# Kernel optimization log

Hardware: AMD Instinct MI355X
Metric: run time of the kernel (lower is better)

## Reference

```python
import jax, jax.numpy as jnp
import numpy as np

CAPS = 16          # num_capsules
DIM = 16           # capsule_dim
NUM_ROUTING = 3
L2_EPS = 1e-12     # tf.nn.l2_normalize epsilon


def setup_inputs() -> dict:
    key = jax.random.key(0)
    k1, k2 = jax.random.split(key)
    inputs = jax.random.normal(k1, (16, 64, 64, 128), dtype=jnp.float32)
    # Conv2D kernel, HWIO layout, fan-in scaled like glorot-ish init
    kernel = jax.random.normal(k2, (3, 3, 128, CAPS * DIM), dtype=jnp.float32) * 0.03
    bias = jnp.zeros((CAPS * DIM,), dtype=jnp.float32)
    return {"inputs": inputs, "kernel": kernel, "bias": bias}


def reference(inputs, kernel, bias):
    # Conv2D(caps*dim, 3x3, padding='same', activation='relu'), channels_last
    x = jax.lax.conv_general_dilated(
        inputs, kernel, window_strides=(1, 1), padding="SAME",
        dimension_numbers=("NHWC", "HWIO", "NHWC"))
    x = jax.nn.relu(x + bias)
    B, H, W, _ = x.shape
    x = x.reshape(B, H * W, CAPS, DIM)            # (B, N, C, D)
    b = jnp.zeros((B, H * W, CAPS), dtype=x.dtype)
    v = None
    for _ in range(NUM_ROUTING):
        c = jax.nn.softmax(b, axis=-1)             # over capsules
        s = jnp.einsum("bnc,bncd->bcd", c, x)      # weighted sum over spatial
        # tf.nn.l2_normalize along last axis
        v = s * jax.lax.rsqrt(jnp.maximum(jnp.sum(s * s, axis=-1, keepdims=True), L2_EPS))
        b = b + jnp.einsum("bncd,bcd->bnc", x, v)  # agreement update
    # tile v over spatial dims: (B,1,1,C*D) -> (B,H,W,C*D)
    out = jnp.broadcast_to(v.reshape(B, 1, 1, CAPS * DIM), (B, H, W, CAPS * DIM))
    return out
```

## Files before the change

kernel.cpp:

```cpp
#include <hip/hip_runtime.h>
#include <hip/hip_bf16.h>

typedef unsigned short u16;
typedef unsigned int   u32;

typedef __bf16 bf16x8 __attribute__((ext_vector_type(8)));
typedef float  f32x4  __attribute__((ext_vector_type(4)));

#define GLDS(gp, lp) __builtin_amdgcn_global_load_lds( \
    (const __attribute__((address_space(1))) void*)(gp), \
    (__attribute__((address_space(3))) void*)(lp), 16, 0, 0)

__device__ __forceinline__ u16 f2b(float f) {
    __hip_bfloat16 h = __float2bfloat16(f);
    u16 u; __builtin_memcpy(&u, &h, 2); return u;
}
__device__ __forceinline__ float blo(u32 u) { return __uint_as_float(u << 16); }
__device__ __forceinline__ float bhi(u32 u) { return __uint_as_float(u & 0xffff0000u); }

__global__ void k_prep(const float* __restrict__ in, const float* __restrict__ wk,
                       u16* __restrict__ pad, u16* __restrict__ BF,
                       float* __restrict__ stats) {
    int bx = blockIdx.x, tid = threadIdx.x;
    if (bx < 4356) {
        int idx = bx * 256 + tid;
        int e0  = idx * 8;
        int ch  = e0 & 127;
        int rest = e0 >> 7;
        int pw = rest % 66;
        int r2 = rest / 66;
        int ph = r2 % 66;
        int b  = r2 / 66;
        u16 ov[8];
        if (ph >= 1 && ph <= 64 && pw >= 1 && pw <= 64) {
            const float* src = in + (((b * 64 + (ph - 1)) * 64 + (pw - 1)) * 128 + ch);
            const float4* s4 = (const float4*)src;
            float4 f0 = s4[0], f1 = s4[1];
            ov[0]=f2b(f0.x); ov[1]=f2b(f0.y); ov[2]=f2b(f0.z); ov[3]=f2b(f0.w);
            ov[4]=f2b(f1.x); ov[5]=f2b(f1.y); ov[6]=f2b(f1.z); ov[7]=f2b(f1.w);
        } else {
            #pragma unroll
            for (int j = 0; j < 8; ++j) ov[j] = 0;
        }
        uint4 w; __builtin_memcpy(&w, ov, 16);
        *(uint4*)(pad + e0) = w;
    } else if (bx < 5508) {
        int t = (bx - 4356) * 256 + tid;
        int j  = t & 7;
        int n  = (t >> 3) & 255;
        int q  = (t >> 11) & 3;
        int kk = (t >> 13) & 3;
        int p  = t >> 15;
        BF[t] = f2b(wk[(p * 128 + kk * 32 + q * 8 + j) * 256 + n]);
    } else {
        stats[(bx - 5508) * 256 + tid] = 0.f;
    }
}

__launch_bounds__(256, 2)
__global__ void k_conv(const u16* __restrict__ Ap, const u16* __restrict__ BF,
                       const float* __restrict__ bias,
                       u16* __restrict__ X, float* __restrict__ s0) {
    __shared__ u16 ldsA[25344];
    const int t = threadIdx.x;
    const int lane = t & 63, wid = t >> 6;
    const int q = lane >> 4, l15 = lane & 15;
    const int bb = blockIdx.x >> 6;
    const int h  = blockIdx.x & 63;
    const int wn0 = wid << 6;

    const int sbase0 = wid * 792;
    #pragma unroll
    for (int i = 0; i < 12; ++i) {
        int sb = sbase0 + i * 64;
        int slot = sb + lane;
        int r = slot / 1056, rem = slot - r * 1056;
        int w = rem >> 4, cs = rem & 15;
        int c = cs ^ (w & 15);
        const u16* g = Ap + ((((bb * 66 + h + r) * 66 + w) << 7) + (c << 3));
        GLDS(g, (char*)ldsA + sb * 16);
    }
    {
        int sb = sbase0 + 768;
        if (lane < 24) {
            int slot = sb + lane;
            int r = slot / 1056, rem = slot - r * 1056;
            int w = rem >> 4, cs = rem & 15;
            int c = cs ^ (w & 15);
            const u16* g = Ap + ((((bb * 66 + h + r) * 66 + w) << 7) + (c << 3));
            GLDS(g, (char*)ldsA + sb * 16);
        }
    }
    __syncthreads();

    const u16* BFl = BF + (q * 2048 + (wn0 + l15) * 8);

    f32x4 zero = {0.f, 0.f, 0.f, 0.f};
    f32x4 acc[4][4];
    #pragma unroll
    for (int mi = 0; mi < 4; ++mi)
        #pragma unroll
        for (int ni = 0; ni < 4; ++ni) acc[mi][ni] = zero;

#define LOADB(B, P) { \
    _Pragma("unroll") for (int kk = 0; kk < 4; ++kk) \
    _Pragma("unroll") for (int ni = 0; ni < 4; ++ni) \
        B[kk * 4 + ni] = *(const bf16x8*)(BFl + (P) * 32768 + kk * 8192 + ni * 128); }

#define COMPP(B, DH, DW) { \
    _Pragma("unroll") for (int kk = 0; kk < 4; ++kk) { \
        bf16x8 af[4]; \
        _Pragma("unroll") for (int mi = 0; mi < 4; ++mi) { \
            int wpos = mi * 16 + l15 + (DW); \
            af[mi] = *(const bf16x8*)((const char*)ldsA + (DH) * 16896 + wpos * 256 + \
                                      (((kk * 4 + q) ^ (wpos & 15)) << 4)); \
        } \
        _Pragma("unroll") for (int mi = 0; mi < 4; ++mi) \
        _Pragma("unroll") for (int ni = 0; ni < 4; ++ni) \
            acc[mi][ni] = __builtin_amdgcn_mfma_f32_16x16x32_bf16( \
                af[mi], B[kk * 4 + ni], acc[mi][ni], 0, 0, 0); } }

    bf16x8 B0[16], B1[16];
    LOADB(B0, 0);
    LOADB(B1, 1); COMPP(B0, 0, 0);
    LOADB(B0, 2); COMPP(B1, 0, 1);
    LOADB(B1, 3); COMPP(B0, 0, 2);
    LOADB(B0, 4); COMPP(B1, 1, 0);
    LOADB(B1, 5); COMPP(B0, 1, 1);
    LOADB(B0, 6); COMPP(B1, 1, 2);
    LOADB(B1, 7); COMPP(B0, 2, 0);
    LOADB(B0, 8); COMPP(B1, 2, 1);
    COMPP(B0, 2, 2);

    float bv[4];
    #pragma unroll
    for (int ni = 0; ni < 4; ++ni) bv[ni] = bias[wn0 + ni * 16 + l15];
    float colsum[4] = {0.f, 0.f, 0.f, 0.f};
    u16* xrow = X + (((bb << 12) + (h << 6) + q * 4) * 256) + wn0 + l15;
    #pragma unroll
    for (int mi = 0; mi < 4; ++mi) {
        #pragma unroll
        for (int rr = 0; rr < 4; ++rr) {
            u16* xp = xrow + (mi * 16 + rr) * 256;
            #pragma unroll
            for (int ni = 0; ni < 4; ++ni) {
                float v = acc[mi][ni][rr] + bv[ni];
                v = v > 0.f ? v : 0.f;
                xp[ni * 16] = f2b(v);
                colsum[ni] += v;
            }
        }
    }
    #pragma unroll
    for (int ni = 0; ni < 4; ++ni) {
        float c = colsum[ni];
        c += __shfl_xor(c, 16);
        c += __shfl_xor(c, 32);
        if (lane < 16) atomicAdd(&s0[bb * 256 + wn0 + ni * 16 + l15], c);
    }
#undef LOADB
#undef COMPP
}

__global__ void k_pass(const u16* __restrict__ X, const float* __restrict__ Sa,
                       const float* __restrict__ Sb, float* __restrict__ Sout,
                       int use2) {
    __shared__ float v1s[256], v2s[256];
    __shared__ float red[4096];
    int t = threadIdx.x, b = blockIdx.y, chunk = blockIdx.x;
    {
        float sa = Sa[b * 256 + t];
        float ss = sa * sa;
        #pragma unroll
        for (int off = 1; off < 16; off <<= 1) ss += __shfl_xor(ss, off);
        ss = ss < 1e-12f ? 1e-12f : ss;
        v1s[t] = sa / sqrtf(ss);
        if (use2) {
            float sb = Sb[b * 256 + t];
            float s2 = sb * sb;
            #pragma unroll
            for (int off = 1; off < 16; off <<= 1) s2 += __shfl_xor(s2, off);
            s2 = s2 < 1e-12f ? 1e-12f : s2;
            v2s[t] = sb / sqrtf(s2);
        } else {
            v2s[t] = 0.f;
        }
    }
    __syncthreads();
    int c = t & 15, nl = t >> 4;
    float acc[16];
    #pragma unroll
    for (int d = 0; d < 16; ++d) acc[d] = 0.f;

    for (int r = 0; r < 8; ++r) {
        int n = chunk * 128 + r * 16 + nl;
        const u16* xp = X + ((b << 12) + n) * 256 + c * 16;
        uint4 a0 = ((const uint4*)xp)[0];
        uint4 a1 = ((const uint4*)xp)[1];
        u32 us[8] = {a0.x, a0.y, a0.z, a0.w, a1.x, a1.y, a1.z, a1.w};
        float xf[16];
        #pragma unroll
        for (int j = 0; j < 8; ++j) { xf[2*j] = blo(us[j]); xf[2*j+1] = bhi(us[j]); }
        float d1 = 0.f, d2 = 0.f;
        #pragma unroll
        for (int d = 0; d < 16; ++d) {
            d1 += xf[d] * v1s[c * 16 + d];
            d2 += xf[d] * v2s[c * 16 + d];
        }
        float bvv = use2 ? (d1 + d2) : d1;
        float mx = bvv;
        #pragma unroll
        for (int off = 1; off < 16; off <<= 1) {
            float o = __shfl_xor(mx, off);
            mx = mx > o ? mx : o;
        }
        float e = expf(bvv - mx);
        float sm = e;
        #pragma unroll
        for (int off = 1; off < 16; off <<= 1) sm += __shfl_xor(sm, off);
        float w = e / sm;
        #pragma unroll
        for (int d = 0; d < 16; ++d) acc[d] += w * xf[d];
    }
    #pragma unroll
    for (int d = 0; d < 16; ++d) red[t * 16 + d] = acc[d];
    __syncthreads();
    int c2 = t >> 4, d2i = t & 15;
    float tot = 0.f;
    #pragma unroll
    for (int n2 = 0; n2 < 16; ++n2) tot += red[(n2 * 16 + c2) * 16 + d2i];
    atomicAdd(&Sout[b * 256 + c2 * 16 + d2i], tot);
}

__global__ void k_bcast(const float* __restrict__ S, float* __restrict__ Out) {
    __shared__ float4 vls[64];
    int t = threadIdx.x, bx = blockIdx.x, b = blockIdx.y;
    float s = S[b * 256 + t];
    float ss = s * s;
    #pragma unroll
    for (int off = 1; off < 16; off <<= 1) ss += __shfl_xor(ss, off);
    ss = ss < 1e-12f ? 1e-12f : ss;
    ((float*)vls)[t] = s / sqrtf(ss);
    __syncthreads();
    float4* o = (float4*)Out + (long)b * 262144 + bx * 8192;
    #pragma unroll
    for (int j = 0; j < 32; ++j) {
        int idx = j * 256 + t;
        o[idx] = vls[idx & 63];
    }
}

extern "C" void kernel_launch(void* const* d_in, const int* in_sizes, int n_in,
                              void* d_out, int out_size, void* d_ws, size_t ws_size,
                              hipStream_t stream) {
    const float* in   = (const float*)d_in[0];
    const float* wk   = (const float*)d_in[1];
    const float* bias = (const float*)d_in[2];
    float* out = (float*)d_out;
    char* ws = (char*)d_ws;

    const size_t OFF_PAD = 0;
    const size_t OFF_BF  = 17842176;
    const size_t OFF_X   = 18432000;
    const size_t OFF_ST  = 51986432;
    const size_t NEEDED  = OFF_ST + 3 * 16384;
    if (ws_size < NEEDED) return;

    u16* pad = (u16*)(ws + OFF_PAD);
    u16* BF  = (u16*)(ws + OFF_BF);
    u16* X   = (u16*)(ws + OFF_X);
    float* s0 = (float*)(ws + OFF_ST);
    float* s2 = s0 + 4096;
    float* s3 = s2 + 4096;

    k_prep <<<5556, 256, 0, stream>>>(in, wk, pad, BF, s0);
    k_conv <<<1024, 256, 0, stream>>>(pad, BF, bias, X, s0);
    k_pass <<<dim3(32, 16), 256, 0, stream>>>(X, s0, s0, s2, 0);
    k_pass <<<dim3(32, 16), 256, 0, stream>>>(X, s0, s2, s3, 1);
    k_bcast<<<dim3(32, 16), 256, 0, stream>>>(s3, out);
}
```

Baseline: 166.5 us.

## Retile conv into 4-row blocks with two-stage channel split staging

Each conv block now computes four output rows across all 256 output channels with 8 waves, instead of one row with 4 waves. The input channels are staged through LDS in two halves of 64, separated by barriers. Fewer halo rows are loaded per output row, so global-to-LDS traffic drops and the LDS buffer is reused across stages. In exchange the grid shrinks to 256 blocks, each wave holds twice the accumulators (a spill risk under the stated launch bounds), and staging does not overlap with compute.

```diff
diff --git a/kernel.cpp b/kernel.cpp
--- a/kernel.cpp
+++ b/kernel.cpp
@@ -57,7 +57,7 @@
     }
 }
 
-__launch_bounds__(256, 2)
+__launch_bounds__(512, 2)
 __global__ void k_conv(const u16* __restrict__ Ap, const u16* __restrict__ BF,
                        const float* __restrict__ bias,
                        u16* __restrict__ X, float* __restrict__ s0) {
@@ -65,80 +65,98 @@
     const int t = threadIdx.x;
     const int lane = t & 63, wid = t >> 6;
     const int q = lane >> 4, l15 = lane & 15;
-    const int bb = blockIdx.x >> 6;
-    const int h  = blockIdx.x & 63;
-    const int wn0 = wid << 6;
-
-    const int sbase0 = wid * 792;
-    #pragma unroll
-    for (int i = 0; i < 12; ++i) {
-        int sb = sbase0 + i * 64;
-        int slot = sb + lane;
-        int r = slot / 1056, rem = slot - r * 1056;
-        int w = rem >> 4, cs = rem & 15;
-        int c = cs ^ (w & 15);
-        const u16* g = Ap + ((((bb * 66 + h + r) * 66 + w) << 7) + (c << 3));
-        GLDS(g, (char*)ldsA + sb * 16);
-    }
-    {
-        int sb = sbase0 + 768;
-        if (lane < 24) {
-            int slot = sb + lane;
-            int r = slot / 1056, rem = slot - r * 1056;
-            int w = rem >> 4, cs = rem & 15;
-            int c = cs ^ (w & 15);
-            const u16* g = Ap + ((((bb * 66 + h + r) * 66 + w) << 7) + (c << 3));
-            GLDS(g, (char*)ldsA + sb * 16);
-        }
-    }
-    __syncthreads();
-
-    const u16* BFl = BF + (q * 2048 + (wn0 + l15) * 8);
-
-    f32x4 zero = {0.f, 0.f, 0.f, 0.f};
-    f32x4 acc[4][4];
-    #pragma unroll
-    for (int mi = 0; mi < 4; ++mi)
-        #pragma unroll
-        for (int ni = 0; ni < 4; ++ni) acc[mi][ni] = zero;
-
-#define LOADB(B, P) { \
-    _Pragma("unroll") for (int kk = 0; kk < 4; ++kk) \
+    const int bb = blockIdx.x >> 4;
+    const int rg = blockIdx.x & 15;
+    const int rg4 = rg << 2;
+    const int wm0 = (wid >> 2) << 7;
+    const int wn0 = (wid & 3) << 6;
+    const int rowb = wm0 >> 6;
+
+#define STAGE(S) { \
+    const int sb0 = wid * 396; \
+    _Pragma("unroll") for (int i = 0; i < 6; ++i) { \
+        int slot = sb0 + i * 64 + lane; \
+        int pr = slot / 528; int rem = slot - pr * 528; \
+        int wp = rem >> 3, cs = rem & 7; \
+        int gc = (S) * 8 + (cs ^ (wp & 7)); \
+        const u16* g = Ap + ((((bb * 66 + rg4 + pr) * 66 + wp) << 7) + (gc << 3)); \
+        GLDS(g, (char*)ldsA + (sb0 + i * 64) * 16); \
+    } \
+    { int slot = sb0 + 384 + lane; \
+      if (lane < 12) { \
+        int pr = slot / 528; int rem = slot - pr * 528; \
+        int wp = rem >> 3, cs = rem & 7; \
+        int gc = (S) * 8 + (cs ^ (wp & 7)); \
+        const u16* g = Ap + ((((bb * 66 + rg4 + pr) * 66 + wp) << 7) + (gc << 3)); \
+        GLDS(g, (char*)ldsA + (sb0 + 384) * 16); \
+      } } }
+
+#define LOADB(B, P, S) { \
+    _Pragma("unroll") for (int kk = 0; kk < 2; ++kk) \
     _Pragma("unroll") for (int ni = 0; ni < 4; ++ni) \
-        B[kk * 4 + ni] = *(const bf16x8*)(BFl + (P) * 32768 + kk * 8192 + ni * 128); }
+        B[kk * 4 + ni] = *(const bf16x8*)(BFl + (P) * 32768 + \
+                                          ((S) * 2 + kk) * 8192 + ni * 128); }
 
 #define COMPP(B, DH, DW) { \
-    _Pragma("unroll") for (int kk = 0; kk < 4; ++kk) { \
-        bf16x8 af[4]; \
-        _Pragma("unroll") for (int mi = 0; mi < 4; ++mi) { \
-            int wpos = mi * 16 + l15 + (DW); \
-            af[mi] = *(const bf16x8*)((const char*)ldsA + (DH) * 16896 + wpos * 256 + \
-                                      (((kk * 4 + q) ^ (wpos & 15)) << 4)); \
+    _Pragma("unroll") for (int kk = 0; kk < 2; ++kk) { \
+        bf16x8 af[8]; \
+        _Pragma("unroll") for (int mi = 0; mi < 8; ++mi) { \
+            int wp = ((mi & 3) << 4) + l15 + (DW); \
+            int pr = rowb + (mi >> 2) + (DH); \
+            int cc = (kk << 2) + q; \
+            af[mi] = *(const bf16x8*)((const char*)ldsA + \
+                ((pr * 528 + (wp << 3) + (cc ^ (wp & 7))) << 4)); \
         } \
-        _Pragma("unroll") for (int mi = 0; mi < 4; ++mi) \
+        _Pragma("unroll") for (int mi = 0; mi < 8; ++mi) \
         _Pragma("unroll") for (int ni = 0; ni < 4; ++ni) \
             acc[mi][ni] = __builtin_amdgcn_mfma_f32_16x16x32_bf16( \
                 af[mi], B[kk * 4 + ni], acc[mi][ni], 0, 0, 0); } }
 
-    bf16x8 B0[16], B1[16];
-    LOADB(B0, 0);
-    LOADB(B1, 1); COMPP(B0, 0, 0);
-    LOADB(B0, 2); COMPP(B1, 0, 1);
-    LOADB(B1, 3); COMPP(B0, 0, 2);
-    LOADB(B0, 4); COMPP(B1, 1, 0);
-    LOADB(B1, 5); COMPP(B0, 1, 1);
-    LOADB(B0, 6); COMPP(B1, 1, 2);
-    LOADB(B1, 7); COMPP(B0, 2, 0);
-    LOADB(B0, 8); COMPP(B1, 2, 1);
+    const u16* BFl = BF + (q * 2048 + (wn0 + l15) * 8);
+
+    f32x4 zero = {0.f, 0.f, 0.f, 0.f};
+    f32x4 acc[8][4];
+    #pragma unroll
+    for (int mi = 0; mi < 8; ++mi)
+        #pragma unroll
+        for (int ni = 0; ni < 4; ++ni) acc[mi][ni] = zero;
+
+    bf16x8 B0[8], B1[8];
+
+    STAGE(0);
+    __syncthreads();
+    LOADB(B0, 0, 0);
+    LOADB(B1, 1, 0); COMPP(B0, 0, 0);
+    LOADB(B0, 2, 0); COMPP(B1, 0, 1);
+    LOADB(B1, 3, 0); COMPP(B0, 0, 2);
+    LOADB(B0, 4, 0); COMPP(B1, 1, 0);
+    LOADB(B1, 5, 0); COMPP(B0, 1, 1);
+    LOADB(B0, 6, 0); COMPP(B1, 1, 2);
+    LOADB(B1, 7, 0); COMPP(B0, 2, 0);
+    LOADB(B0, 8, 0); COMPP(B1, 2, 1);
+    COMPP(B0, 2, 2);
+    __syncthreads();
+
+    STAGE(1);
+    __syncthreads();
+    LOADB(B0, 0, 1);
+    LOADB(B1, 1, 1); COMPP(B0, 0, 0);
+    LOADB(B0, 2, 1); COMPP(B1, 0, 1);
+    LOADB(B1, 3, 1); COMPP(B0, 0, 2);
+    LOADB(B0, 4, 1); COMPP(B1, 1, 0);
+    LOADB(B1, 5, 1); COMPP(B0, 1, 1);
+    LOADB(B0, 6, 1); COMPP(B1, 1, 2);
+    LOADB(B1, 7, 1); COMPP(B0, 2, 0);
+    LOADB(B0, 8, 1); COMPP(B1, 2, 1);
     COMPP(B0, 2, 2);
 
     float bv[4];
     #pragma unroll
     for (int ni = 0; ni < 4; ++ni) bv[ni] = bias[wn0 + ni * 16 + l15];
     float colsum[4] = {0.f, 0.f, 0.f, 0.f};
-    u16* xrow = X + (((bb << 12) + (h << 6) + q * 4) * 256) + wn0 + l15;
-    #pragma unroll
-    for (int mi = 0; mi < 4; ++mi) {
+    u16* xrow = X + (((bb << 12) + (rg << 8) + wm0 + q * 4) * 256) + wn0 + l15;
+    #pragma unroll
+    for (int mi = 0; mi < 8; ++mi) {
         #pragma unroll
         for (int rr = 0; rr < 4; ++rr) {
             u16* xp = xrow + (mi * 16 + rr) * 256;
@@ -158,6 +176,7 @@
         c += __shfl_xor(c, 32);
         if (lane < 16) atomicAdd(&s0[bb * 256 + wn0 + ni * 16 + l15], c);
     }
+#undef STAGE
 #undef LOADB
 #undef COMPP
 }
@@ -274,7 +293,7 @@
     float* s3 = s2 + 4096;
 
     k_prep <<<5556, 256, 0, stream>>>(in, wk, pad, BF, s0);
-    k_conv <<<1024, 256, 0, stream>>>(pad, BF, bias, X, s0);
+    k_conv <<<256, 512, 0, stream>>>(pad, BF, bias, X, s0);
     k_pass <<<dim3(32, 16), 256, 0, stream>>>(X, s0, s0, s2, 0);
     k_pass <<<dim3(32, 16), 256, 0, stream>>>(X, s0, s2, s3, 1);
     k_bcast<<<dim3(32, 16), 256, 0, stream>>>(s3, out);
```

Result: slower. 183.6 us (+10.3%).
